# Optimization experiments

Hardware: AMD Instinct MI355X
Metric: run time of the kernel (lower is better)

The kernel has to match this reference:

```python
import jax, jax.numpy as jnp
import numpy as np
from jax.scipy.special import logsumexp

B, N = 256, 65536
NEG_INF = jnp.float32(-1e30)  # acts as -inf for logsumexp, keeps grads finite


def setup_inputs() -> dict:
    key = jax.random.key(0)
    k1, k2 = jax.random.split(key)
    sim = jax.random.uniform(k1, (B, N), dtype=jnp.float32)
    label = jax.random.uniform(k2, (B, N), dtype=jnp.float32)
    return {"sim": sim, "label": label}


def _ranking_loss(sim, label):
    m = 0.2
    gamma = 64.0
    delta_p = 1.0 - m  # 0.8
    delta_n = m        # 0.2

    pos_mask = label > 0.5
    neg_mask = label < 0.25

    # ---- positives: logit_p = -relu(0.8 - sim).detach() * (sim - 0.8) * gamma ----
    alpha_p = jax.lax.stop_gradient(jnp.maximum(0.8 - sim, 0.0))
    logit_p = -alpha_p * (sim - delta_p) * gamma
    lse_p = logsumexp(jnp.where(pos_mask, logit_p, NEG_INF), axis=1)
    # torch fallback: no positives -> logit_p = [0.0], logsumexp == 0
    lse_p = jnp.where(pos_mask.any(axis=1), lse_p, 0.0)

    # ---- negatives: if >20 negatives, keep only top-10 largest sims ----
    alpha_n_all = jax.lax.stop_gradient(jnp.maximum(sim - 0.2, 0.0))
    logit_n_all = alpha_n_all * (sim - delta_n) * gamma
    lse_n_all = logsumexp(jnp.where(neg_mask, logit_n_all, NEG_INF), axis=1)

    neg_sim_masked = jnp.where(neg_mask, sim, NEG_INF)
    top_v, _ = jax.lax.top_k(neg_sim_masked, 10)  # [B, 10]
    alpha_n_top = jax.lax.stop_gradient(jnp.maximum(top_v - 0.2, 0.0))
    logit_n_top = alpha_n_top * (top_v - delta_n) * gamma
    lse_n_top = logsumexp(logit_n_top, axis=1)

    n_neg = neg_mask.sum(axis=1)
    lse_n = jnp.where(n_neg > 20, lse_n_top, lse_n_all)

    loss_loc = jax.nn.softplus(lse_n + lse_p).sum()
    return loss_loc / sim.shape[0]  # reduction='mean'


def reference(sim, label):
    return _ranking_loss(sim, label)
```

## Files before the change

### kernel.cpp

```cpp
#include <hip/hip_runtime.h>
#include <cmath>

#define NEG_INF (-1.0e30f)

static constexpr int B = 256;
static constexpr int N = 65536;
static constexpr int THREADS = 1024;
static constexpr int SPLIT = 2;
static constexpr float C_OFF = 40.96f;

__device__ __forceinline__ float wave_sum_f(float v) {
#pragma unroll
  for (int off = 32; off >= 1; off >>= 1) v += __shfl_xor(v, off, 64);
  return v;
}
__device__ __forceinline__ int wave_sum_i(int v) {
#pragma unroll
  for (int off = 32; off >= 1; off >>= 1) v += __shfl_xor(v, off, 64);
  return v;
}

__device__ __forceinline__ void merge_lists_shfl(float t[16], int off) {
  float b[16];
#pragma unroll
  for (int i = 0; i < 16; ++i) b[i] = __shfl_xor(t[i], off, 64);
  float c[16];
#pragma unroll
  for (int i = 0; i < 16; ++i) c[i] = fmaxf(t[i], b[15 - i]);
#pragma unroll
  for (int s = 8; s >= 1; s >>= 1) {
#pragma unroll
    for (int i = 0; i < 16; ++i) {
      if ((i & s) == 0) {
        float lo = c[i], hi = c[i + s];
        c[i] = fmaxf(lo, hi);
        c[i + s] = fminf(lo, hi);
      }
    }
  }
#pragma unroll
  for (int i = 0; i < 16; ++i) t[i] = c[i];
}

__device__ __forceinline__ void merge_lists_local(float a[16], const float b[16]) {
  float c[16];
#pragma unroll
  for (int i = 0; i < 16; ++i) c[i] = fmaxf(a[i], b[15 - i]);
#pragma unroll
  for (int s = 8; s >= 1; s >>= 1) {
#pragma unroll
    for (int i = 0; i < 16; ++i) {
      if ((i & s) == 0) {
        float lo = c[i], hi = c[i + s];
        c[i] = fmaxf(lo, hi);
        c[i + s] = fminf(lo, hi);
      }
    }
  }
#pragma unroll
  for (int i = 0; i < 16; ++i) a[i] = c[i];
}

__device__ __forceinline__ void process_elem(float s, float l, float& s_p,
                                             float& s_n, int& nn, float t[16]) {
  const bool pos = l > 0.5f;
  const bool neg = l < 0.25f;
  float d = pos ? (0.8f - s) : (s - 0.2f);
  float r = fmaxf(d, 0.f);
  float arg = __builtin_fmaf(64.f * r, r, -C_OFF);
  float e = __expf(arg);
  if (pos) s_p += e;
  if (neg) {
    s_n += e;
    ++nn;
    if (s > t[9]) {
      t[9] = s;
#pragma unroll
      for (int i = 9; i > 0; --i) {
        float a = t[i - 1], bb = t[i];
        t[i - 1] = fmaxf(a, bb);
        t[i] = fminf(a, bb);
      }
    }
  }
}

__global__ void __launch_bounds__(THREADS, 8) ranking_partial_kernel(
    const float* __restrict__ sim, const float* __restrict__ label,
    float* __restrict__ ws_sp, float* __restrict__ ws_sn,
    int* __restrict__ ws_cnt, float* __restrict__ ws_top) {
  const int blk = blockIdx.x;
  const int row = blk >> 1;
  const int half = blk & 1;
  const int tid = threadIdx.x;
  const size_t base4 = (size_t)row * (N / 4) + (size_t)half * (N / (4 * SPLIT));
  const float4* sim4 = reinterpret_cast<const float4*>(sim) + base4;
  const float4* lab4 = reinterpret_cast<const float4*>(label) + base4;

  float s_p = 0.f, s_n = 0.f;
  int nn = 0;
  float t[16];
#pragma unroll
  for (int i = 0; i < 16; ++i) t[i] = NEG_INF;

  constexpr int ITER = N / 4 / THREADS / SPLIT;
#pragma unroll
  for (int it = 0; it < ITER; ++it) {
    float4 sv = sim4[it * THREADS + tid];
    float4 lv = lab4[it * THREADS + tid];
    process_elem(sv.x, lv.x, s_p, s_n, nn, t);
    process_elem(sv.y, lv.y, s_p, s_n, nn, t);
    process_elem(sv.z, lv.z, s_p, s_n, nn, t);
    process_elem(sv.w, lv.w, s_p, s_n, nn, t);
  }

  s_p = wave_sum_f(s_p);
  s_n = wave_sum_f(s_n);
  nn = wave_sum_i(nn);
#pragma unroll
  for (int off = 1; off < 64; off <<= 1) merge_lists_shfl(t, off);

  __shared__ float ls_p[16], ls_n[16];
  __shared__ int ls_c[16];
  __shared__ float ltop[16][16];
  const int wave = tid >> 6, lane = tid & 63;
  if (lane == 0) {
    ls_p[wave] = s_p;
    ls_n[wave] = s_n;
    ls_c[wave] = nn;
#pragma unroll
    for (int i = 0; i < 16; ++i) ltop[wave][i] = t[i];
  }
  __syncthreads();

  if (wave == 0) {
    float m[16];
    if (lane < 16) {
#pragma unroll
      for (int i = 0; i < 16; ++i) m[i] = ltop[lane][i];
    } else {
#pragma unroll
      for (int i = 0; i < 16; ++i) m[i] = NEG_INF;
    }
    merge_lists_shfl(m, 1);
    merge_lists_shfl(m, 2);
    merge_lists_shfl(m, 4);
    merge_lists_shfl(m, 8);

    float sp = (lane < 16) ? ls_p[lane] : 0.f;
    float sn = (lane < 16) ? ls_n[lane] : 0.f;
    int cn = (lane < 16) ? ls_c[lane] : 0;
    sp = wave_sum_f(sp);
    sn = wave_sum_f(sn);
    cn = wave_sum_i(cn);

    if (lane == 0) {
      ws_sp[blk] = sp;
      ws_sn[blk] = sn;
      ws_cnt[blk] = cn;
#pragma unroll
      for (int i = 0; i < 16; ++i) ws_top[blk * 16 + i] = m[i];
    }
  }
}

__global__ void __launch_bounds__(256) combine_kernel(
    const float* __restrict__ ws_sp, const float* __restrict__ ws_sn,
    const int* __restrict__ ws_cnt, const float* __restrict__ ws_top,
    float* __restrict__ out) {
  const int r = threadIdx.x;
  const int p0 = r * 2, p1 = r * 2 + 1;

  float a[16], b[16];
#pragma unroll
  for (int i = 0; i < 16; ++i) a[i] = ws_top[p0 * 16 + i];
#pragma unroll
  for (int i = 0; i < 16; ++i) b[i] = ws_top[p1 * 16 + i];
  merge_lists_local(a, b);

  float sp = ws_sp[p0] + ws_sp[p1];
  float sn = ws_sn[p0] + ws_sn[p1];
  int cn = ws_cnt[p0] + ws_cnt[p1];

  float lse_p = (sp > 0.f) ? (C_OFF + __logf(sp)) : 0.f;
  float lse_n_all = (sn > 0.f) ? (C_OFF + __logf(sn)) : NEG_INF;

  float mx = NEG_INF;
  float lg[10];
#pragma unroll
  for (int i = 0; i < 10; ++i) {
    float v = a[i];
    float al = fmaxf(v - 0.2f, 0.f);
    float lo = al * (v - 0.2f) * 64.f;
    lg[i] = lo;
    mx = fmaxf(mx, lo);
  }
  float ss = 0.f;
#pragma unroll
  for (int i = 0; i < 10; ++i) ss += __expf(lg[i] - mx);
  float lse_n_top = mx + __logf(ss);

  float lse_n = (cn > 20) ? lse_n_top : lse_n_all;
  float x = lse_n + lse_p;
  float loss = fmaxf(x, 0.f) + log1pf(__expf(-fabsf(x)));

  float v = wave_sum_f(loss);
  __shared__ float wsh[4];
  if ((r & 63) == 0) wsh[r >> 6] = v;
  __syncthreads();
  if (r == 0) out[0] = (wsh[0] + wsh[1] + wsh[2] + wsh[3]) * (1.0f / 256.0f);
}

extern "C" void kernel_launch(void* const* d_in, const int* in_sizes, int n_in,
                              void* d_out, int out_size, void* d_ws, size_t ws_size,
                              hipStream_t stream) {
  const float* sim = (const float*)d_in[0];
  const float* label = (const float*)d_in[1];
  float* out = (float*)d_out;

  float* wsf = (float*)d_ws;
  float* ws_sp = wsf;
  float* ws_sn = wsf + 512;
  float* ws_top = wsf + 1024;
  int* ws_cnt = (int*)(wsf + 1024 + 512 * 16);

  ranking_partial_kernel<<<dim3(B * SPLIT), dim3(THREADS), 0, stream>>>(
      sim, label, ws_sp, ws_sn, ws_cnt, ws_top);
  combine_kernel<<<dim3(1), dim3(256), 0, stream>>>(ws_sp, ws_sn, ws_cnt, ws_top,
                                                    out);
}
```

Before: 162.7 us.

## Use smaller blocks with 4-way row split and batched float4 loads

Blocks shrink from 1024 to 256 threads and each row is split across 4 blocks instead of 2. Each thread now issues four float4 loads of sim and label before processing them, which raises memory-level parallelism. The combine kernel merges SPLIT partial top-k lists and sums per row, and the workspace layout is parameterised by the block count. Each thread now handles 64 elements instead of 32. The extra loaded registers may lower occupancy, and the combine step does more merging per row.

Result: no change. 161.5 us (-0.8%).

```diff
diff --git a/kernel.cpp b/kernel.cpp
--- a/kernel.cpp
+++ b/kernel.cpp
@@ -5,8 +5,8 @@
 
 static constexpr int B = 256;
 static constexpr int N = 65536;
-static constexpr int THREADS = 1024;
-static constexpr int SPLIT = 2;
+static constexpr int THREADS = 256;
+static constexpr int SPLIT = 4;
 static constexpr float C_OFF = 40.96f;
 
 __device__ __forceinline__ float wave_sum_f(float v) {
@@ -85,15 +85,15 @@
   }
 }
 
-__global__ void __launch_bounds__(THREADS, 8) ranking_partial_kernel(
+__global__ void __launch_bounds__(THREADS, 4) ranking_partial_kernel(
     const float* __restrict__ sim, const float* __restrict__ label,
     float* __restrict__ ws_sp, float* __restrict__ ws_sn,
     int* __restrict__ ws_cnt, float* __restrict__ ws_top) {
   const int blk = blockIdx.x;
-  const int row = blk >> 1;
-  const int half = blk & 1;
+  const int row = blk >> 2;
+  const int part = blk & 3;
   const int tid = threadIdx.x;
-  const size_t base4 = (size_t)row * (N / 4) + (size_t)half * (N / (4 * SPLIT));
+  const size_t base4 = (size_t)row * (N / 4) + (size_t)part * (N / (4 * SPLIT));
   const float4* sim4 = reinterpret_cast<const float4*>(sim) + base4;
   const float4* lab4 = reinterpret_cast<const float4*>(label) + base4;
 
@@ -105,13 +105,20 @@
 
   constexpr int ITER = N / 4 / THREADS / SPLIT;
 #pragma unroll
-  for (int it = 0; it < ITER; ++it) {
-    float4 sv = sim4[it * THREADS + tid];
-    float4 lv = lab4[it * THREADS + tid];
-    process_elem(sv.x, lv.x, s_p, s_n, nn, t);
-    process_elem(sv.y, lv.y, s_p, s_n, nn, t);
-    process_elem(sv.z, lv.z, s_p, s_n, nn, t);
-    process_elem(sv.w, lv.w, s_p, s_n, nn, t);
+  for (int it = 0; it < ITER; it += 4) {
+    float4 sv[4], lv[4];
+#pragma unroll
+    for (int j = 0; j < 4; ++j) {
+      sv[j] = sim4[(it + j) * THREADS + tid];
+      lv[j] = lab4[(it + j) * THREADS + tid];
+    }
+#pragma unroll
+    for (int j = 0; j < 4; ++j) {
+      process_elem(sv[j].x, lv[j].x, s_p, s_n, nn, t);
+      process_elem(sv[j].y, lv[j].y, s_p, s_n, nn, t);
+      process_elem(sv[j].z, lv[j].z, s_p, s_n, nn, t);
+      process_elem(sv[j].w, lv[j].w, s_p, s_n, nn, t);
+    }
   }
 
   s_p = wave_sum_f(s_p);
@@ -120,9 +127,9 @@
 #pragma unroll
   for (int off = 1; off < 64; off <<= 1) merge_lists_shfl(t, off);
 
-  __shared__ float ls_p[16], ls_n[16];
-  __shared__ int ls_c[16];
-  __shared__ float ltop[16][16];
+  __shared__ float ls_p[4], ls_n[4];
+  __shared__ int ls_c[4];
+  __shared__ float ltop[4][16];
   const int wave = tid >> 6, lane = tid & 63;
   if (lane == 0) {
     ls_p[wave] = s_p;
@@ -135,7 +142,7 @@
 
   if (wave == 0) {
     float m[16];
-    if (lane < 16) {
+    if (lane < 4) {
 #pragma unroll
       for (int i = 0; i < 16; ++i) m[i] = ltop[lane][i];
     } else {
@@ -144,12 +151,10 @@
     }
     merge_lists_shfl(m, 1);
     merge_lists_shfl(m, 2);
-    merge_lists_shfl(m, 4);
-    merge_lists_shfl(m, 8);
-
-    float sp = (lane < 16) ? ls_p[lane] : 0.f;
-    float sn = (lane < 16) ? ls_n[lane] : 0.f;
-    int cn = (lane < 16) ? ls_c[lane] : 0;
+
+    float sp = (lane < 4) ? ls_p[lane] : 0.f;
+    float sn = (lane < 4) ? ls_n[lane] : 0.f;
+    int cn = (lane < 4) ? ls_c[lane] : 0;
     sp = wave_sum_f(sp);
     sn = wave_sum_f(sn);
     cn = wave_sum_i(cn);
@@ -169,18 +174,27 @@
     const int* __restrict__ ws_cnt, const float* __restrict__ ws_top,
     float* __restrict__ out) {
   const int r = threadIdx.x;
-  const int p0 = r * 2, p1 = r * 2 + 1;
-
-  float a[16], b[16];
+  const int p0 = r * SPLIT;
+
+  float a[16];
 #pragma unroll
   for (int i = 0; i < 16; ++i) a[i] = ws_top[p0 * 16 + i];
 #pragma unroll
-  for (int i = 0; i < 16; ++i) b[i] = ws_top[p1 * 16 + i];
-  merge_lists_local(a, b);
-
-  float sp = ws_sp[p0] + ws_sp[p1];
-  float sn = ws_sn[p0] + ws_sn[p1];
-  int cn = ws_cnt[p0] + ws_cnt[p1];
+  for (int k = 1; k < SPLIT; ++k) {
+    float b[16];
+#pragma unroll
+    for (int i = 0; i < 16; ++i) b[i] = ws_top[(p0 + k) * 16 + i];
+    merge_lists_local(a, b);
+  }
+
+  float sp = 0.f, sn = 0.f;
+  int cn = 0;
+#pragma unroll
+  for (int k = 0; k < SPLIT; ++k) {
+    sp += ws_sp[p0 + k];
+    sn += ws_sn[p0 + k];
+    cn += ws_cnt[p0 + k];
+  }
 
   float lse_p = (sp > 0.f) ? (C_OFF + __logf(sp)) : 0.f;
   float lse_n_all = (sn > 0.f) ? (C_OFF + __logf(sn)) : NEG_INF;
@@ -218,13 +232,14 @@
   const float* label = (const float*)d_in[1];
   float* out = (float*)d_out;
 
+  constexpr int P = B * SPLIT;
   float* wsf = (float*)d_ws;
   float* ws_sp = wsf;
-  float* ws_sn = wsf + 512;
-  float* ws_top = wsf + 1024;
-  int* ws_cnt = (int*)(wsf + 1024 + 512 * 16);
-
-  ranking_partial_kernel<<<dim3(B * SPLIT), dim3(THREADS), 0, stream>>>(
+  float* ws_sn = wsf + P;
+  float* ws_top = wsf + 2 * P;
+  int* ws_cnt = (int*)(wsf + 2 * P + P * 16);
+
+  ranking_partial_kernel<<<dim3(P), dim3(THREADS), 0, stream>>>(
       sim, label, ws_sp, ws_sn, ws_cnt, ws_top);
   combine_kernel<<<dim3(1), dim3(256), 0, stream>>>(ws_sp, ws_sn, ws_cnt, ws_top,
                                                     out);
```
